# Kernel optimization log

Hardware: AMD Instinct MI355X
Metric: run time of the kernel (lower is better)

The kernel has to match this reference:

```python
import jax, jax.numpy as jnp
import numpy as np

NUM_HEADS = 16
KEY_DIM = 128
VALUE_DIM = 128
HIDDEN = 2048


def setup_inputs() -> dict:
    key = jax.random.key(0)
    k1, k2, k3 = jax.random.split(key, 3)
    B, T = 4, 2048
    hidden_states = jax.random.normal(k1, (B, T, HIDDEN), dtype=jnp.float32)
    # qkv_proj: Linear(hidden, H*(2*key_dim+value_dim)) no bias -> weight (out, in)
    qkv_out = NUM_HEADS * (2 * KEY_DIM + VALUE_DIM)
    w_qkv = jax.random.normal(k2, (qkv_out, HIDDEN), dtype=jnp.float32) * (1.0 / np.sqrt(HIDDEN))
    w_out = jax.random.normal(k3, (HIDDEN, NUM_HEADS * VALUE_DIM), dtype=jnp.float32) * (1.0 / np.sqrt(NUM_HEADS * VALUE_DIM))
    b_out = jnp.zeros((HIDDEN,), dtype=jnp.float32)
    return {"hidden_states": hidden_states, "w_qkv": w_qkv, "w_out": w_out, "b_out": b_out}


def reference(hidden_states, w_qkv, w_out, b_out):
    B, T, _ = hidden_states.shape
    H, Dk, Dv = NUM_HEADS, KEY_DIM, VALUE_DIM
    scale = 1.0 / np.sqrt(Dk).astype(np.float32)
    qkv = hidden_states @ w_qkv.T  # (B,T,H*(2Dk+Dv))
    q, k, v = jnp.split(qkv, [H * Dk, 2 * H * Dk], axis=-1)
    q = q.reshape(B, T, H, Dk).transpose(0, 2, 1, 3)  # (B,H,T,Dk)
    k = k.reshape(B, T, H, Dk).transpose(0, 2, 1, 3)
    v = v.reshape(B, T, H, Dv).transpose(0, 2, 1, 3)
    scores = jnp.einsum('bhtd,bhsd->bhts', q, k) * scale  # (B,H,T,S)
    causal = jnp.tril(jnp.ones((T, T), dtype=bool))
    scores = jnp.where(causal[None, None], scores, jnp.float32(-jnp.inf))
    attn = jax.nn.softmax(scores, axis=-1)
    out = jnp.einsum('bhts,bhsd->bhtd', attn, v)  # (B,H,T,Dv)
    out = out.transpose(0, 2, 1, 3).reshape(B, T, H * Dv)
    return out @ w_out.T + b_out
```

## Files before the change

kernel.cpp:

```cpp
#include <hip/hip_runtime.h>
#include <hip/hip_bf16.h>
#include <stdint.h>

#define HID   2048
#define NH    16
#define QKV_N 6144
#define BT    8192
#define TT    2048

typedef short bf16x8  __attribute__((ext_vector_type(8)));
typedef float f32x4   __attribute__((ext_vector_type(4)));
typedef float f32x16  __attribute__((ext_vector_type(16)));
typedef unsigned short u16;

__device__ __forceinline__ u16 f2bf(float f){
  union { float f; unsigned u; } v; v.f = f;
  unsigned r = 0x7fffu + ((v.u >> 16) & 1u);
  return (u16)((v.u + r) >> 16);
}
__device__ __forceinline__ float bf2f(u16 x){
  union { unsigned u; float f; } v; v.u = ((unsigned)x) << 16;
  return v.f;
}
__device__ __forceinline__ unsigned cvt_pk_bf16(float lo, float hi){
  unsigned r;
  asm("v_cvt_pk_bf16_f32 %0, %1, %2" : "=v"(r) : "v"(lo), "v"(hi));
  return r;
}

typedef __attribute__((address_space(3))) void lds_vt;
typedef const __attribute__((address_space(1))) void gbl_vt;

__device__ __forceinline__ void gload16(const void* g, void* l){
  __builtin_amdgcn_global_load_lds((gbl_vt*)g, (lds_vt*)l, 16, 0, 0);
}

#define FENCE() asm volatile("" ::: "memory")
#define SYNC()  { FENCE(); __builtin_amdgcn_s_barrier(); FENCE(); }

__global__ __launch_bounds__(256) void cvt_bf16(const float* __restrict__ in,
                                                u16* __restrict__ out, int n4){
  int i = blockIdx.x * blockDim.x + threadIdx.x;
  int stride = gridDim.x * blockDim.x;
  for (; i < n4; i += stride){
    float4 v = ((const float4*)in)[i];
    ushort4 o;
    o.x = f2bf(v.x); o.y = f2bf(v.y); o.z = f2bf(v.z); o.w = f2bf(v.w);
    ((ushort4*)out)[i] = o;
  }
}

template<int OUT_BF16>
__global__ __launch_bounds__(512, 2) void gemm256(const u16* __restrict__ A,
                                                  const u16* __restrict__ Bm,
                                                  u16* __restrict__ Cb,
                                                  float* __restrict__ Cf,
                                                  const float* __restrict__ bias,
                                                  int M, int N, int K)
{
  __shared__ u16 lds[4 * 256 * 64];
  u16* const Abuf[2] = { lds,          lds + 16384 };
  u16* const Bbuf[2] = { lds + 32768,  lds + 49152 };

  const int tid  = threadIdx.x;
  const int w    = tid >> 6;
  const int lane = tid & 63;
  const int wm   = w >> 2;
  const int wn   = w & 3;
  const int l31  = lane & 31;
  const int hi   = lane >> 5;
  const int sw7  = l31 & 7;

  int bid = blockIdx.x;
  { int qq = gridDim.x >> 3; bid = (bid & 7) * qq + (bid >> 3); }
  const int ntile = N >> 8;
  const int m0 = (bid / ntile) << 8;
  const int n0 = (bid % ntile) << 8;

  const int rS = tid >> 3;
  const int cS = ((tid & 7) ^ (rS & 7)) * 8;
  const u16* gA = A  + (size_t)(m0 + rS) * K + cS;
  const u16* gB = Bm + (size_t)(n0 + rS) * K + cS;
  const int wds = w * 512;

  f32x16 acc[4][2] = {};
  bf16x8 aq[2][4], bq[2][4];

  auto stgA = [&](int buf, int half, int kt){
    const u16* s = gA + (size_t)(half * 128) * K + (size_t)kt * 64;
    gload16(s,                  Abuf[buf] + half * 8192 + wds);
    gload16(s + (size_t)64 * K, Abuf[buf] + half * 8192 + 4096 + wds);
  };
  auto stgB = [&](int buf, int half, int kt){
    const u16* s = gB + (size_t)(half * 128) * K + (size_t)kt * 64;
    gload16(s,                  Bbuf[buf] + half * 8192 + wds);
    gload16(s + (size_t)64 * K, Bbuf[buf] + half * 8192 + 4096 + wds);
  };
  auto loadA = [&](const u16* ab, int mp){
    #pragma unroll
    for (int mi = 0; mi < 2; ++mi){
      const int row = wm * 128 + (mp * 2 + mi) * 32 + l31;
      #pragma unroll
      for (int ks = 0; ks < 4; ++ks){
        const int blk = (ks * 2 + hi) ^ sw7;
        aq[mi][ks] = *(const bf16x8*)(ab + row * 64 + blk * 8);
      }
    }
  };
  auto loadB = [&](const u16* bb){
    #pragma unroll
    for (int ni = 0; ni < 2; ++ni){
      const int row = wn * 64 + ni * 32 + l31;
      #pragma unroll
      for (int ks = 0; ks < 4; ++ks){
        const int blk = (ks * 2 + hi) ^ sw7;
        bq[ni][ks] = *(const bf16x8*)(bb + row * 64 + blk * 8);
      }
    }
  };

#define MFMAP(MP) do {                                                        \
    __builtin_amdgcn_s_setprio(1);                                            \
    _Pragma("unroll")                                                         \
    for (int ks = 0; ks < 4; ++ks){                                           \
      _Pragma("unroll")                                                       \
      for (int mi = 0; mi < 2; ++mi){                                         \
        _Pragma("unroll")                                                     \
        for (int ni = 0; ni < 2; ++ni)                                        \
          acc[(MP)*2+mi][ni] = __builtin_amdgcn_mfma_f32_32x32x16_bf16(       \
              aq[mi][ks], bq[ni][ks], acc[(MP)*2+mi][ni], 0, 0, 0);           \
      }                                                                       \
    }                                                                         \
    __builtin_amdgcn_s_setprio(0);                                            \
  } while (0)

  stgA(0, 0, 0); stgA(0, 1, 0);
  stgB(0, 0, 0); stgB(0, 1, 0);
  stgB(1, 0, 1); stgB(1, 1, 1);
  asm volatile("s_waitcnt vmcnt(4)" ::: "memory");
  SYNC();

  const int NI = K >> 7;
  for (int it = 0; it < NI; ++it){
    const int t = it * 2;
    const bool lastI = (it == NI - 1);

    loadB(Bbuf[0]);
    loadA(Abuf[0], 0);
    stgA(1, 0, t + 1); stgA(1, 1, t + 1);
    SYNC(); MFMAP(0); SYNC();
    loadA(Abuf[0], 1);
    if (!lastI){ stgB(0, 0, t + 2); stgB(0, 1, t + 2); }
    SYNC(); MFMAP(1);
    if (lastI) asm volatile("s_waitcnt vmcnt(0)" ::: "memory");
    else       asm volatile("s_waitcnt vmcnt(4)" ::: "memory");
    SYNC();

    loadB(Bbuf[1]);
    loadA(Abuf[1], 0);
    if (!lastI){ stgA(0, 0, t + 2); stgA(0, 1, t + 2); }
    SYNC(); MFMAP(0); SYNC();
    loadA(Abuf[1], 1);
    if (!lastI){ stgB(1, 0, t + 3); stgB(1, 1, t + 3); }
    SYNC(); MFMAP(1);
    if (!lastI) asm volatile("s_waitcnt vmcnt(4)" ::: "memory");
    SYNC();
  }
#undef MFMAP

  #pragma unroll
  for (int mt = 0; mt < 4; ++mt)
    #pragma unroll
    for (int nt = 0; nt < 2; ++nt){
      const int col = n0 + wn * 64 + nt * 32 + l31;
      const float bs = OUT_BF16 ? 0.f : bias[col];
      #pragma unroll
      for (int r = 0; r < 16; ++r){
        const int row = m0 + wm * 128 + mt * 32 + (r & 3) + 8 * (r >> 2) + 4 * hi;
        const float v = acc[mt][nt][r];
        if (OUT_BF16)
          Cb[(size_t)row * N + col] = f2bf(v);
        else
          Cf[(size_t)row * N + col] = v + bs;
      }
    }
}

__global__ __launch_bounds__(256) void vtrans(const u16* __restrict__ qkv,
                                              u16* __restrict__ vt2){
  __shared__ u16 tile[32][136];
  const int t5 = blockIdx.x;
  const int bh = blockIdx.y;
  const int b = bh >> 4, h = bh & 15;
  const int tid = threadIdx.x;

  #pragma unroll
  for (int p = 0; p < 2; ++p){
    int idx = p * 256 + tid;
    int row = idx >> 4;
    int c8  = (idx & 15) * 8;
    bf16x8 v = *(const bf16x8*)(qkv + (size_t)(b * TT + t5 * 32 + row) * QKV_N + 4096 + h * 128 + c8);
    *(bf16x8*)(&tile[row][c8]) = v;
  }
  __syncthreads();
  u16* outp = vt2 + (size_t)(bh * 64 + t5) * 4096;
  #pragma unroll
  for (int p = 0; p < 2; ++p){
    int id = p * 256 + tid;
    int r  = id >> 3;
    int sp = id & 7;
    int sl = sp ^ (r & 7);
    int d  = (sl >> 2) * 64 + r;
    int kv = (sl & 3) * 8;
    bf16x8 v;
    #pragma unroll
    for (int e = 0; e < 8; ++e) v[e] = (short)tile[kv + e][d];
    *(bf16x8*)(outp + id * 8) = v;
  }
}

__global__ __launch_bounds__(256, 3) void attn(const u16* __restrict__ qkv,
                                               const u16* __restrict__ vt2,
                                               u16* __restrict__ aout)
{
  __shared__ u16 Kl[3][32 * 128];
  __shared__ u16 Vl[3][64 * 64];

  const int qt = 15 - (int)blockIdx.y;
  const int bh = blockIdx.x;
  const int b = bh >> 4, h = bh & 15;
  const int tid  = threadIdx.x;
  const int w    = tid >> 6;
  const int lane = tid & 63;
  const int l31  = lane & 31;
  const int hi   = lane >> 5;
  const int sw7  = l31 & 7;

  const int qg = qt * 128 + w * 32 + l31;
  const float sc2 = 0.08838834764831845f * 1.4426950408889634f;

  bf16x8 qf[8];
  {
    const u16* qp = qkv + (size_t)(b * TT + qg) * QKV_N + h * 128 + hi * 8;
    #pragma unroll
    for (int s = 0; s < 8; ++s){
      bf16x8 raw = *(const bf16x8*)(qp + s * 16);
      unsigned pk[4];
      #pragma unroll
      for (int p2 = 0; p2 < 4; ++p2)
        pk[p2] = cvt_pk_bf16(bf2f((u16)raw[2 * p2]) * sc2,
                             bf2f((u16)raw[2 * p2 + 1]) * sc2);
      int4 u = { (int)pk[0], (int)pk[1], (int)pk[2], (int)pk[3] };
      qf[s] = *(bf16x8*)&u;
    }
  }

  f32x16 o[4] = {};
  float lsum = 0.f;

  const u16* ksrc = qkv + (size_t)(b * TT + (tid >> 4)) * QKV_N + 2048 + h * 128
                    + (((tid & 15) ^ ((tid >> 4) & 7)) * 8);
  const u16* vsrc = vt2 + (size_t)bh * (64 * 4096) + tid * 8;

  auto stage = [&](int buf, int j){
    const u16* ks = ksrc + (size_t)(j * 32) * QKV_N;
    gload16(ks,                      &Kl[buf][tid * 8]);
    gload16(ks + (size_t)16 * QKV_N, &Kl[buf][2048 + tid * 8]);
    const u16* vs = vsrc + (size_t)j * 4096;
    gload16(vs,        &Vl[buf][tid * 8]);
    gload16(vs + 2048, &Vl[buf][2048 + tid * 8]);
  };

  const int NT  = 4 * qt + 4;
  const int jme = qt * 4 + w;
  stage(0, 0);
  stage(1, 1);

  int cur = 0;
  for (int j = 0; j < NT; ++j){
    SYNC();
    if (j + 2 < NT){
      int nb = cur + 2; if (nb >= 3) nb -= 3;
      stage(nb, j + 2);
      asm volatile("s_waitcnt vmcnt(8)" ::: "memory");
    } else if (j + 1 < NT){
      asm volatile("s_waitcnt vmcnt(4)" ::: "memory");
    } else {
      asm volatile("s_waitcnt vmcnt(0)" ::: "memory");
    }
    SYNC();

    if (j <= jme){
      f32x16 sa = {}, sb = {};
      const u16* KB = Kl[cur];
      __builtin_amdgcn_s_setprio(1);
      #pragma unroll
      for (int sl = 0; sl < 4; ++sl){
        const int spa = ((sl * 2 + hi) ^ sw7) * 8;
        const int spb = (((sl + 4) * 2 + hi) ^ sw7) * 8;
        bf16x8 ka = *(const bf16x8*)(KB + l31 * 128 + spa);
        bf16x8 kb2 = *(const bf16x8*)(KB + l31 * 128 + spb);
        sa = __builtin_amdgcn_mfma_f32_32x32x16_bf16(ka,  qf[sl],     sa, 0, 0, 0);
        sb = __builtin_amdgcn_mfma_f32_32x32x16_bf16(kb2, qf[sl + 4], sb, 0, 0, 0);
      }
      __builtin_amdgcn_s_setprio(0);

      f32x16 s;
      #pragma unroll
      for (int r = 0; r < 16; ++r) s[r] = sa[r] + sb[r];

      if (j == jme){
        #pragma unroll
        for (int r = 0; r < 16; ++r){
          const int krow = (r & 3) + 8 * (r >> 2) + 4 * hi;
          if (krow > l31) s[r] = -3.0e38f;
        }
      }

      #pragma unroll
      for (int r = 0; r < 16; ++r) s[r] = exp2f(s[r]);
      {
        float t0 = (s[0] + s[1]) + (s[2] + s[3]);
        float t1 = (s[4] + s[5]) + (s[6] + s[7]);
        float t2 = (s[8] + s[9]) + (s[10] + s[11]);
        float t3 = (s[12] + s[13]) + (s[14] + s[15]);
        lsum += (t0 + t1) + (t2 + t3);
      }

      bf16x8 pf[2];
      #pragma unroll
      for (int kb = 0; kb < 2; ++kb){
        const int R0 = kb * 8;
        const unsigned wa0 = cvt_pk_bf16(s[R0],     s[R0 + 1]);
        const unsigned wa1 = cvt_pk_bf16(s[R0 + 2], s[R0 + 3]);
        const unsigned wb0 = cvt_pk_bf16(s[R0 + 4], s[R0 + 5]);
        const unsigned wb1 = cvt_pk_bf16(s[R0 + 6], s[R0 + 7]);
        const int s0 = hi ? (int)wa0 : (int)wb0;
        const int s1 = hi ? (int)wa1 : (int)wb1;
        const int r0 = __shfl_xor(s0, 32, 64);
        const int r1 = __shfl_xor(s1, 32, 64);
        int4 u;
        u.x = hi ? r0 : (int)wa0;
        u.y = hi ? r1 : (int)wa1;
        u.z = hi ? (int)wb0 : r0;
        u.w = hi ? (int)wb1 : r1;
        pf[kb] = *(bf16x8*)&u;
      }

      const u16* VB = Vl[cur];
      __builtin_amdgcn_s_setprio(1);
      #pragma unroll
      for (int db = 0; db < 4; ++db){
        const int r6 = (db & 1) * 32 + l31;
        const int hd = db >> 1;
        #pragma unroll
        for (int kb = 0; kb < 2; ++kb){
          const int sp = ((hd * 4 + kb * 2 + hi) ^ sw7) * 8;
          bf16x8 vf = *(const bf16x8*)(VB + r6 * 64 + sp);
          o[db] = __builtin_amdgcn_mfma_f32_32x32x16_bf16(vf, pf[kb], o[db], 0, 0, 0);
        }
      }
      __builtin_amdgcn_s_setprio(0);
    }

    ++cur; if (cur == 3) cur = 0;
  }

  const float lt = lsum + __shfl_xor(lsum, 32, 64);
  const float inv = 1.0f / lt;
  u16* op = aout + (size_t)(b * TT + qg) * HID + h * 128;
  #pragma unroll
  for (int db = 0; db < 4; ++db)
    #pragma unroll
    for (int rq = 0; rq < 4; ++rq){
      ushort4 pk;
      pk.x = f2bf(o[db][rq * 4 + 0] * inv);
      pk.y = f2bf(o[db][rq * 4 + 1] * inv);
      pk.z = f2bf(o[db][rq * 4 + 2] * inv);
      pk.w = f2bf(o[db][rq * 4 + 3] * inv);
      *(ushort4*)(op + db * 32 + rq * 8 + hi * 4) = pk;
    }
}

extern "C" void kernel_launch(void* const* d_in, const int* in_sizes, int n_in,
                              void* d_out, int out_size, void* d_ws, size_t ws_size,
                              hipStream_t stream)
{
  (void)in_sizes; (void)n_in; (void)out_size; (void)ws_size;
  const float* hs    = (const float*)d_in[0];
  const float* w_qkv = (const float*)d_in[1];
  const float* w_out = (const float*)d_in[2];
  const float* b_out = (const float*)d_in[3];
  float* out = (float*)d_out;

  char* ws = (char*)d_ws;
  u16* qkv_bf  = (u16*)(ws);
  u16* wout_bf = (u16*)(ws + 100663296);
  u16* hs_bf   = (u16*)(ws + 109051904);
  u16* attn_bf = hs_bf;
  u16* wqkv_bf = (u16*)(ws + 142606336);
  u16* vt2_bf  = wqkv_bf;

  cvt_bf16<<<2048, 256, 0, stream>>>(hs,    hs_bf,   (BT * HID) / 4);
  cvt_bf16<<<2048, 256, 0, stream>>>(w_qkv, wqkv_bf, (QKV_N * HID) / 4);
  cvt_bf16<<<1024, 256, 0, stream>>>(w_out, wout_bf, (HID * 2048) / 4);

  gemm256<1><<<(BT / 256) * (QKV_N / 256), 512, 0, stream>>>(
      hs_bf, wqkv_bf, qkv_bf, nullptr, nullptr, BT, QKV_N, HID);

  vtrans<<<dim3(TT / 32, 64), 256, 0, stream>>>(qkv_bf, vt2_bf);

  attn<<<dim3(64, 16), 256, 0, stream>>>(qkv_bf, vt2_bf, attn_bf);

  gemm256<0><<<(BT / 256) * (HID / 256), 512, 0, stream>>>(
      attn_bf, wout_bf, nullptr, out, b_out, BT, HID, HID);
}
```

Measured before the change: 406.0 us.

## Fuse conversion kernels and reorganize GEMM LDS tile layout into 16-row subtiles

Merges the three fp32-to-bf16 conversion launches into a single kernel that dispatches by index range, removing two launches and their tail gaps. The bf16 GEMM staging is remapped so each 32-row MFMA fragment is stored as 16-row by 32-k sub-blocks with a new XOR swizzle, and the LDS fragment reads are changed to match. The new layout aims to reduce LDS bank conflicts or improve global-load coalescing, at the cost of more complex index math and a risk of mismatched staging and read addressing.

```diff
diff --git a/kernel.cpp b/kernel.cpp
--- a/kernel.cpp
+++ b/kernel.cpp
@@ -38,15 +38,21 @@
 #define FENCE() asm volatile("" ::: "memory")
 #define SYNC()  { FENCE(); __builtin_amdgcn_s_barrier(); FENCE(); }
 
-__global__ __launch_bounds__(256) void cvt_bf16(const float* __restrict__ in,
-                                                u16* __restrict__ out, int n4){
+__global__ __launch_bounds__(256) void cvt_all(const float* __restrict__ in1, u16* __restrict__ o1, int n1,
+                                               const float* __restrict__ in2, u16* __restrict__ o2, int n2,
+                                               const float* __restrict__ in3, u16* __restrict__ o3, int n3){
   int i = blockIdx.x * blockDim.x + threadIdx.x;
-  int stride = gridDim.x * blockDim.x;
-  for (; i < n4; i += stride){
-    float4 v = ((const float4*)in)[i];
+  const int stride = gridDim.x * blockDim.x;
+  const int ntot = n1 + n2 + n3;
+  for (; i < ntot; i += stride){
+    const float* ip; u16* op; int k;
+    if (i < n1)            { ip = in1; op = o1; k = i; }
+    else if (i < n1 + n2)  { ip = in2; op = o2; k = i - n1; }
+    else                   { ip = in3; op = o3; k = i - n1 - n2; }
+    float4 v = ((const float4*)ip)[k];
     ushort4 o;
     o.x = f2bf(v.x); o.y = f2bf(v.y); o.z = f2bf(v.z); o.w = f2bf(v.w);
-    ((ushort4*)out)[i] = o;
+    ((ushort4*)op)[k] = o;
   }
 }
 
@@ -70,6 +76,8 @@
   const int l31  = lane & 31;
   const int hi   = lane >> 5;
   const int sw7  = l31 & 7;
+  const int r15  = l31 & 15;
+  const int sbase = (l31 >> 4) | (hi << 1);
 
   int bid = blockIdx.x;
   { int qq = gridDim.x >> 3; bid = (bid & 7) * qq + (bid >> 3); }
@@ -77,44 +85,53 @@
   const int m0 = (bid / ntile) << 8;
   const int n0 = (bid % ntile) << 8;
 
-  const int rS = tid >> 3;
-  const int cS = ((tid & 7) ^ (rS & 7)) * 8;
-  const u16* gA = A  + (size_t)(m0 + rS) * K + cS;
-  const u16* gB = Bm + (size_t)(n0 + rS) * K + cS;
+  int rowS[2], kS[2];
+  #pragma unroll
+  for (int i = 0; i < 2; ++i){
+    int tt  = i * 512 + tid;
+    int sub = (tt >> 8) & 3;
+    int rg  = (tt >> 7) & 1;
+    int r   = (tt >> 3) & 15;
+    int sl  = (tt & 7) ^ (r & 7);
+    rowS[i] = sub * 32 + (sl & 1) * 16 + r;
+    kS[i]   = (((rg << 1) | (sl >> 2)) << 4) + ((sl >> 1) & 1) * 8;
+  }
+  const u16* gA0 = A  + (size_t)(m0 + rowS[0]) * K + kS[0];
+  const u16* gA1 = A  + (size_t)(m0 + rowS[1]) * K + kS[1];
+  const u16* gB0 = Bm + (size_t)(n0 + rowS[0]) * K + kS[0];
+  const u16* gB1 = Bm + (size_t)(n0 + rowS[1]) * K + kS[1];
   const int wds = w * 512;
 
   f32x16 acc[4][2] = {};
   bf16x8 aq[2][4], bq[2][4];
 
   auto stgA = [&](int buf, int half, int kt){
-    const u16* s = gA + (size_t)(half * 128) * K + (size_t)kt * 64;
-    gload16(s,                  Abuf[buf] + half * 8192 + wds);
-    gload16(s + (size_t)64 * K, Abuf[buf] + half * 8192 + 4096 + wds);
+    gload16(gA0 + (size_t)(half * 128) * K + kt * 64, Abuf[buf] + half * 8192 + wds);
+    gload16(gA1 + (size_t)(half * 128) * K + kt * 64, Abuf[buf] + half * 8192 + 4096 + wds);
   };
   auto stgB = [&](int buf, int half, int kt){
-    const u16* s = gB + (size_t)(half * 128) * K + (size_t)kt * 64;
-    gload16(s,                  Bbuf[buf] + half * 8192 + wds);
-    gload16(s + (size_t)64 * K, Bbuf[buf] + half * 8192 + 4096 + wds);
+    gload16(gB0 + (size_t)(half * 128) * K + kt * 64, Bbuf[buf] + half * 8192 + wds);
+    gload16(gB1 + (size_t)(half * 128) * K + kt * 64, Bbuf[buf] + half * 8192 + 4096 + wds);
   };
   auto loadA = [&](const u16* ab, int mp){
     #pragma unroll
     for (int mi = 0; mi < 2; ++mi){
-      const int row = wm * 128 + (mp * 2 + mi) * 32 + l31;
+      const u16* base = ab + (wm * 4 + mp * 2 + mi) * 2048 + r15 * 64;
       #pragma unroll
       for (int ks = 0; ks < 4; ++ks){
-        const int blk = (ks * 2 + hi) ^ sw7;
-        aq[mi][ks] = *(const bf16x8*)(ab + row * 64 + blk * 8);
+        const int slot = (sbase | ((ks & 1) << 2)) ^ sw7;
+        aq[mi][ks] = *(const bf16x8*)(base + (ks >> 1) * 1024 + slot * 8);
       }
     }
   };
   auto loadB = [&](const u16* bb){
     #pragma unroll
     for (int ni = 0; ni < 2; ++ni){
-      const int row = wn * 64 + ni * 32 + l31;
+      const u16* base = bb + (wn * 2 + ni) * 2048 + r15 * 64;
       #pragma unroll
       for (int ks = 0; ks < 4; ++ks){
-        const int blk = (ks * 2 + hi) ^ sw7;
-        bq[ni][ks] = *(const bf16x8*)(bb + row * 64 + blk * 8);
+        const int slot = (sbase | ((ks & 1) << 2)) ^ sw7;
+        bq[ni][ks] = *(const bf16x8*)(base + (ks >> 1) * 1024 + slot * 8);
       }
     }
   };
@@ -401,9 +418,9 @@
   u16* wqkv_bf = (u16*)(ws + 142606336);
   u16* vt2_bf  = wqkv_bf;
 
-  cvt_bf16<<<2048, 256, 0, stream>>>(hs,    hs_bf,   (BT * HID) / 4);
-  cvt_bf16<<<2048, 256, 0, stream>>>(w_qkv, wqkv_bf, (QKV_N * HID) / 4);
-  cvt_bf16<<<1024, 256, 0, stream>>>(w_out, wout_bf, (HID * 2048) / 4);
+  cvt_all<<<4096, 256, 0, stream>>>(hs,    hs_bf,   (BT * HID) / 4,
+                                    w_qkv, wqkv_bf, (QKV_N * HID) / 4,
+                                    w_out, wout_bf, (HID * 2048) / 4);
 
   gemm256<1><<<(BT / 256) * (QKV_N / 256), 512, 0, stream>>>(
       hs_bf, wqkv_bf, qkv_bf, nullptr, nullptr, BT, QKV_N, HID);
```

Result: faster. 388.1 us (-4.4%).
